# Optimization experiments

Measured on AMD Instinct MI355X. Metric: run time of the kernel, lower is better.

## Reference

```python
import jax, jax.numpy as jnp
import numpy as np

B, S, T, D = 8, 8, 256, 256          # batch, series, time_steps, input_dim
H, DK = 8, 64                         # attn_heads, attn_dim
HD = H * DK                           # 512
L = 2                                 # attn_layers
F = 256                               # mlp_dim
R = 512                               # resolution
M = 128                               # number of mid-points sampled this step
EPS = 1e-5


def setup_inputs() -> dict:
    key = jax.random.key(0)
    ks = iter(jax.random.split(key, 64))

    def rn(shape, scale=0.05):
        return scale * jax.random.normal(next(ks), shape, dtype=jnp.float32)

    inp = {
        'encoded': jax.random.normal(next(ks), (B, S, T, D), dtype=jnp.float32),
        'true_u': jax.random.uniform(next(ks), (B, S, T), dtype=jnp.float32),
        'mid_idx': jnp.sort(jax.random.randint(next(ks), (M,), 0, T)),
        'left_idx': jax.random.randint(next(ks), (M,), 0, T),
        'right_idx': jax.random.randint(next(ks), (M,), 0, T),
        'i': 3,
        # dimension_shift
        'ds_W': rn((D, HD)), 'ds_b': jnp.zeros((HD,), jnp.float32),
        # per-layer, per-head key-creator MLPs (stacked): (D+1) -> F -> F -> DK
        'kW1': rn((L, H, D + 1, F)), 'kb1': jnp.zeros((L, H, F), jnp.float32),
        'kW2': rn((L, H, F, F)),     'kb2': jnp.zeros((L, H, F), jnp.float32),
        'kW3': rn((L, H, F, DK)),    'kb3': jnp.zeros((L, H, DK), jnp.float32),
        # value-creator MLPs
        'vW1': rn((L, H, D + 1, F)), 'vb1': jnp.zeros((L, H, F), jnp.float32),
        'vW2': rn((L, H, F, F)),     'vb2': jnp.zeros((L, H, F), jnp.float32),
        'vW3': rn((L, H, F, DK)),    'vb3': jnp.zeros((L, H, DK), jnp.float32),
        # attention / feed-forward layer norms
        'ln1_g': jnp.ones((L, HD), jnp.float32), 'ln1_b': jnp.zeros((L, HD), jnp.float32),
        'ln2_g': jnp.ones((L, HD), jnp.float32), 'ln2_b': jnp.zeros((L, HD), jnp.float32),
        # feed-forwards
        'ffW1': rn((L, HD, HD)), 'ffb1': jnp.zeros((L, HD), jnp.float32),
        'ffW2': rn((L, HD, HD)), 'ffb2': jnp.zeros((L, HD), jnp.float32),
        # dist_extractors MLP: HD -> F -> F -> R
        'deW1': rn((HD, F)), 'deb1': jnp.zeros((F,), jnp.float32),
        'deW2': rn((F, F)),  'deb2': jnp.zeros((F,), jnp.float32),
        'deW3': rn((F, R)),  'deb3': jnp.zeros((R,), jnp.float32),
    }
    return inp


def _mlp_heads(x, W1, b1, W2, b2, W3, b3):
    # x: [B,S,T,D+1]; weights: [L,H,...] -> out [L,B,S,T,H,DK]
    h = jax.nn.relu(jnp.einsum('bstc,lhcf->lbsthf', x, W1) + b1[:, None, None, None])
    h = jax.nn.relu(jnp.einsum('lbsthf,lhfg->lbsthg', h, W2) + b2[:, None, None, None])
    return jnp.einsum('lbsthg,lhgd->lbsthd', h, W3) + b3[:, None, None, None]


def _ln(x, g, b):
    mu = jnp.mean(x, axis=-1, keepdims=True)
    var = jnp.mean(jnp.square(x - mu), axis=-1, keepdims=True)
    return (x - mu) * jax.lax.rsqrt(var + EPS) * g + b


def reference(encoded, true_u, mid_idx, left_idx, right_idx, i,
              ds_W, ds_b,
              kW1, kb1, kW2, kb2, kW3, kb3,
              vW1, vb1, vW2, vb2, vW3, vb3,
              ln1_g, ln1_b, ln2_g, ln2_b,
              ffW1, ffb1, ffW2, ffb2,
              deW1, deb1, deW2, deb2, deW3, deb3):
    # merged_input = cat([encoded, true_u[..., None]])  -> [B,S,T,D+1]
    merged = jnp.concatenate([encoded, true_u[..., None]], axis=-1)

    keys = _mlp_heads(merged, kW1, kb1, kW2, kb2, kW3, kb3)   # [L,B,S,T,H,DK]
    values = _mlp_heads(merged, vW1, vb1, vW2, vb2, vW3, vb3)  # [L,B,S,T,H,DK]

    srange = jnp.arange(S)
    # n=1 neighbor: time index = loop counter m for series < i, else right[m]
    # (faithful to keys_hist[:, :i, mid:mid+1] in the original)
    idx1 = jnp.where(srange[None, :] < i, jnp.arange(M)[:, None], right_idx[:, None])  # [M,S]

    def gather_neighbors(kv):  # kv: [L,B,S,T,H,DK] -> [L,B,M,S,2,H,DK]
        n0 = jnp.transpose(kv[:, :, :, left_idx], (0, 1, 3, 2, 4, 5))  # [L,B,M,S,H,DK]
        n1 = kv[:, :, srange[None, :], idx1]                            # [L,B,M,S,H,DK]
        return jnp.stack([n0, n1], axis=4)

    nk = gather_neighbors(keys)
    nv = gather_neighbors(values)

    pred = encoded[:, i, mid_idx]                  # [B,M,D]
    att_value = pred @ ds_W + ds_b                 # [B,M,HD]

    scale = DK ** (-0.5)
    for l in range(L):
        avh = att_value.reshape(B, M, H, DK)
        prod = jnp.einsum('bmhd,bmsnhd->bmhsn', avh, nk[l]) * scale
        w = jax.nn.softmax(prod, axis=-1)          # softmax over n only, as in source
        att = jnp.einsum('bmhsn,bmsnhd->bmhd', w, nv[l]).reshape(B, M, HD)
        x = _ln(att_value + att, ln1_g[l], ln1_b[l])
        ff = jax.nn.relu(x @ ffW1[l] + ffb1[l]) @ ffW2[l] + ffb2[l]
        att_value = _ln(x + ff, ln2_g[l], ln2_b[l])

    h = jax.nn.relu(att_value @ deW1 + deb1)
    h = jax.nn.relu(h @ deW2 + deb2)
    logits = h @ deW3 + deb3                       # [B,M,R]
    return logits
```

## Files before the change

### kernel.cpp

```cpp
#include <hip/hip_runtime.h>
#include <hip/hip_bf16.h>

#define NB 8
#define NS 8
#define NT 256
#define ND 256
#define NH 8
#define NDK 64
#define NHD 512
#define NL 2
#define NF 256
#define NR 512
#define NM 128
#define NTOK 16384
#define NROW 1024

typedef __attribute__((ext_vector_type(8))) short short8;
typedef __attribute__((ext_vector_type(4))) float f32x4;

__device__ __forceinline__ unsigned short f2bf(float x) {
    unsigned u = __builtin_bit_cast(unsigned, x);
    unsigned r = (u + 0x7fffu + ((u >> 16) & 1u)) >> 16;
    return (unsigned short)r;
}
__device__ __forceinline__ float bf2f(unsigned short x) {
    return __builtin_bit_cast(float, ((unsigned)x) << 16);
}
__device__ __forceinline__ float wred(float v) {
#pragma unroll
    for (int o = 32; o > 0; o >>= 1) v += __shfl_xor(v, o, 64);
    return v;
}

__global__ __launch_bounds__(256) void prep_all(
    const float* __restrict__ enc,
    const float* __restrict__ kW1, const float* __restrict__ kW2, const float* __restrict__ kW3,
    const float* __restrict__ vW1, const float* __restrict__ vW2, const float* __restrict__ vW3,
    const float* __restrict__ dsW, const float* __restrict__ ffW1,
    const float* __restrict__ ffW2, const float* __restrict__ deW1,
    const float* __restrict__ deW2, const float* __restrict__ deW3,
    unsigned short* __restrict__ XF, unsigned short* __restrict__ WP,
    float* __restrict__ W1L, unsigned short* __restrict__ WG) {
    __shared__ float T[32][257];
    int bid = blockIdx.x, tid = threadIdx.x;
    if (bid < 512) {
        int t0 = bid * 32;
        const float* src = enc + (size_t)t0 * 256;
#pragma unroll
        for (int it = 0; it < 8; ++it) {
            int f4 = it * 256 + tid;
            int row = f4 >> 6, c = (f4 & 63) * 4;
            float4 v = *(const float4*)(src + row * 256 + c);
            T[row][c] = v.x; T[row][c + 1] = v.y; T[row][c + 2] = v.z; T[row][c + 3] = v.w;
        }
        __syncthreads();
        int tile = t0 >> 7, g = (t0 >> 6) & 1, nt0 = (t0 >> 4) & 3;
#pragma unroll
        for (int i = 0; i < 32; i += 8) {
            int o = tid * 32 + i;
            int lane = (o >> 3) & 63, ntp = (o >> 9) & 1, kc = o >> 10;
            int id = lane & 15, quad = lane >> 4;
            __align__(16) unsigned short p[8];
#pragma unroll
            for (int j = 0; j < 8; ++j) p[j] = f2bf(T[ntp * 16 + id][kc * 32 + quad * 8 + j]);
            size_t dsto = ((size_t)((((tile * 8 + kc) * 2 + g) * 4 + (nt0 + ntp)) * 64 + lane)) * 8;
            *(uint4*)(XF + dsto) = *(uint4*)p;
        }
    } else if (bid < 1280) {
        int lb = bid - 512;
        int combo = lb / 24, r = lb % 24;
        int st = r >> 3, kc = r & 7;
        int kvv = combo >> 4, l = (combo >> 3) & 1, h = combo & 7;
        unsigned short* dstc = WP + (size_t)combo * 147456;
        if (st < 2) {
            const float* W = (st == 0) ? (kvv ? vW1 : kW1) : (kvv ? vW2 : kW2);
            int rows = (st == 0) ? 257 : 256;
            const float* src = W + ((size_t)(l * 8 + h) * rows + kc * 32) * 256;
#pragma unroll
            for (int it = 0; it < 8; ++it) {
                int f4 = it * 256 + tid;
                int row = f4 >> 6, c = (f4 & 63) * 4;
                float4 v = *(const float4*)(src + (size_t)row * 256 + c);
                T[row][c] = v.x; T[row][c + 1] = v.y; T[row][c + 2] = v.z; T[row][c + 3] = v.w;
            }
            __syncthreads();
            unsigned short* dst = dstc + st * 65536 + kc * 8192;
#pragma unroll
            for (int i = 0; i < 32; i += 8) {
                int o = tid * 32 + i;
                int lane = (o >> 3) & 63, ftile = o >> 9;
                int id = lane & 15, quad = lane >> 4;
                __align__(16) unsigned short p[8];
#pragma unroll
                for (int j = 0; j < 8; ++j) p[j] = f2bf(T[quad * 8 + j][ftile * 16 + id]);
                *(uint4*)(dst + o) = *(uint4*)p;
            }
            if (st == 0 && kc == 0) {
                const float* hw = (kvv ? vW1 : kW1) + (size_t)(l * 8 + h) * 257 * 256;
                W1L[combo * 256 + tid] = hw[65536 + tid];
            }
        } else {
            const float* src = (kvv ? vW3 : kW3) + ((size_t)(l * 8 + h) * 256 + kc * 32) * 64;
#pragma unroll
            for (int it = 0; it < 2; ++it) {
                int f4 = it * 256 + tid;
                int row = f4 >> 4, c = (f4 & 15) * 4;
                float4 v = *(const float4*)(src + (size_t)row * 64 + c);
                T[row][c] = v.x; T[row][c + 1] = v.y; T[row][c + 2] = v.z; T[row][c + 3] = v.w;
            }
            __syncthreads();
            unsigned short* dst = dstc + 131072 + kc * 2048;
            int o = tid * 8;
            int lane = tid & 63, ftile = tid >> 6;
            int id = lane & 15, quad = lane >> 4;
            __align__(16) unsigned short p[8];
#pragma unroll
            for (int j = 0; j < 8; ++j) p[j] = f2bf(T[quad * 8 + j][ftile * 16 + id]);
            *(uint4*)(dst + o) = *(uint4*)p;
        }
    } else {
        int lb0 = bid - 1280;
        const float* src; int N, kc, ng; size_t base;
        if (lb0 < 32)       { int lb = lb0;       src = dsW;           N = 512; base = 0;       kc = lb >> 2; ng = lb & 3; }
        else if (lb0 < 96)  { int lb = lb0 - 32;  src = ffW1;          N = 512; base = 131072;  kc = lb >> 2; ng = lb & 3; }
        else if (lb0 < 160) { int lb = lb0 - 96;  src = ffW1 + 262144; N = 512; base = 393216;  kc = lb >> 2; ng = lb & 3; }
        else if (lb0 < 224) { int lb = lb0 - 160; src = ffW2;          N = 512; base = 655360;  kc = lb >> 2; ng = lb & 3; }
        else if (lb0 < 288) { int lb = lb0 - 224; src = ffW2 + 262144; N = 512; base = 917504;  kc = lb >> 2; ng = lb & 3; }
        else if (lb0 < 320) { int lb = lb0 - 288; src = deW1;          N = 256; base = 1179648; kc = lb >> 1; ng = lb & 1; }
        else if (lb0 < 336) { int lb = lb0 - 320; src = deW2;          N = 256; base = 1310720; kc = lb >> 1; ng = lb & 1; }
        else                { int lb = lb0 - 336; src = deW3;          N = 512; base = 1376256; kc = lb >> 2; ng = lb & 3; }
        int NTl = N >> 4;
        const float* s = src + (size_t)(kc * 32) * N + ng * 128;
#pragma unroll
        for (int it = 0; it < 4; ++it) {
            int f4 = it * 256 + tid;
            int row = f4 >> 5, c = (f4 & 31) * 4;
            float4 v = *(const float4*)(s + (size_t)row * N + c);
            T[row][c] = v.x; T[row][c + 1] = v.y; T[row][c + 2] = v.z; T[row][c + 3] = v.w;
        }
        __syncthreads();
        unsigned short* d = WG + base + (size_t)(kc * NTl + ng * 8) * 512;
#pragma unroll
        for (int i = 0; i < 16; i += 8) {
            int o = tid * 16 + i;
            int lane = (o >> 3) & 63, ntl = o >> 9;
            int id = lane & 15, quad = lane >> 4;
            __align__(16) unsigned short p[8];
#pragma unroll
            for (int j = 0; j < 8; ++j) p[j] = f2bf(T[quad * 8 + j][ntl * 16 + id]);
            *(uint4*)(d + o) = *(uint4*)p;
        }
    }
}

__global__ __launch_bounds__(256, 4) void heads_mlp(
    const float* __restrict__ tu, const unsigned short* __restrict__ XF,
    const unsigned short* __restrict__ WP, const float* __restrict__ W1L,
    const float* __restrict__ kb1, const float* __restrict__ kb2, const float* __restrict__ kb3,
    const float* __restrict__ vb1, const float* __restrict__ vb2, const float* __restrict__ vb3,
    unsigned short* __restrict__ KV) {
    __shared__ __align__(16) unsigned short smem[16896];

    const int tid = threadIdx.x;
    const int w2 = tid >> 6, lane = tid & 63, id = lane & 15, quad = lane >> 4;
    const int bx = blockIdx.x;
    const int xcd = bx & 7;
    const int idx = bx >> 3;
    const int combo = xcd * 4 + (idx & 3);
    const int t64 = idx >> 2;
    const int kvv = combo >> 4, l = (combo >> 3) & 1, h = combo & 7;
    const int r0 = t64 * 64;
    const int tile128 = t64 >> 1, g = t64 & 1;
    const unsigned short* WF1 = WP + (size_t)combo * 147456;
    const unsigned short* WF2 = WF1 + 65536;
    const unsigned short* WF3 = WF1 + 131072;
    const float* b1 = (kvv ? vb1 : kb1) + (l * 8 + h) * 256;
    const float* b2 = (kvv ? vb2 : kb2) + (l * 8 + h) * 256;
    const float* b3 = (kvv ? vb3 : kb3) + (l * 8 + h) * 64;

    short8 afb[2][4];
#pragma unroll
    for (int ft = 0; ft < 4; ++ft) {
        afb[0][ft] = *(const short8*)(WF1 + (size_t)((w2 * 4 + ft) * 64 + lane) * 8);
        afb[1][ft] = *(const short8*)(WF1 + (size_t)((16 + w2 * 4 + ft) * 64 + lane) * 8);
    }
    {
        const uint4* s = (const uint4*)(XF + (size_t)tile128 * 32768 + g * 2048);
        uint4* d = (uint4*)smem;
#pragma unroll
        for (int kc = 0; kc < 8; ++kc) d[kc * 256 + tid] = s[kc * 512 + tid];
    }
    __syncthreads();

    f32x4 acc[4][4];
#pragma unroll
    for (int i = 0; i < 4; ++i)
#pragma unroll
        for (int j = 0; j < 4; ++j) acc[i][j] = (f32x4){0.f, 0.f, 0.f, 0.f};

    {
#pragma unroll
        for (int kc = 0; kc < 8; ++kc) {
            short8 tn[4];
            if (kc + 2 < 8) {
#pragma unroll
                for (int ft = 0; ft < 4; ++ft)
                    tn[ft] = *(const short8*)(WF1 + (size_t)(((kc + 2) * 16 + w2 * 4 + ft) * 64 + lane) * 8);
            }
            short8 bf[4];
#pragma unroll
            for (int nt = 0; nt < 4; ++nt)
                bf[nt] = *(const short8*)(smem + (size_t)(kc * 4 + nt) * 512 + lane * 8);
#pragma unroll
            for (int ft = 0; ft < 4; ++ft)
#pragma unroll
                for (int nt = 0; nt < 4; ++nt)
                    acc[ft][nt] = __builtin_amdgcn_mfma_f32_16x16x32_bf16(afb[kc & 1][ft], bf[nt], acc[ft][nt], 0, 0, 0);
            if (kc + 2 < 8) {
#pragma unroll
                for (int ft = 0; ft < 4; ++ft) afb[kc & 1][ft] = tn[ft];
            }
        }
    }
    __syncthreads();
    {
        float ur[4];
#pragma unroll
        for (int nt = 0; nt < 4; ++nt) ur[nt] = tu[r0 + nt * 16 + id];
#pragma unroll
        for (int ft = 0; ft < 4; ++ft) {
            int fb = w2 * 64 + ft * 16 + quad * 4;
            float4 bb = *(const float4*)(b1 + fb);
            float4 wl = *(const float4*)(W1L + combo * 256 + fb);
            const float* bbp = (const float*)&bb;
            const float* wlp = (const float*)&wl;
#pragma unroll
            for (int nt = 0; nt < 4; ++nt) {
                unsigned short p[4];
#pragma unroll
                for (int r = 0; r < 4; ++r) {
                    float v = acc[ft][nt][r] + bbp[r] + ur[nt] * wlp[r];
                    p[r] = f2bf(fmaxf(v, 0.f));
                }
                uint2 pk;
                pk.x = (unsigned)p[0] | ((unsigned)p[1] << 16);
                pk.y = (unsigned)p[2] | ((unsigned)p[3] << 16);
                *(uint2*)(smem + (size_t)(nt * 16 + id) * 264 + fb) = pk;
            }
        }
    }
    __syncthreads();

#pragma unroll
    for (int i = 0; i < 4; ++i)
#pragma unroll
        for (int j = 0; j < 4; ++j) acc[i][j] = (f32x4){0.f, 0.f, 0.f, 0.f};
    {
#pragma unroll
        for (int ft = 0; ft < 4; ++ft) {
            afb[0][ft] = *(const short8*)(WF2 + (size_t)((w2 * 4 + ft) * 64 + lane) * 8);
            afb[1][ft] = *(const short8*)(WF2 + (size_t)((16 + w2 * 4 + ft) * 64 + lane) * 8);
        }
#pragma unroll
        for (int kc = 0; kc < 8; ++kc) {
            short8 tn[4];
            if (kc + 2 < 8) {
#pragma unroll
                for (int ft = 0; ft < 4; ++ft)
                    tn[ft] = *(const short8*)(WF2 + (size_t)(((kc + 2) * 16 + w2 * 4 + ft) * 64 + lane) * 8);
            }
            short8 bf[4];
#pragma unroll
            for (int nt = 0; nt < 4; ++nt)
                bf[nt] = *(const short8*)(smem + (size_t)(nt * 16 + id) * 264 + kc * 32 + quad * 8);
#pragma unroll
            for (int ft = 0; ft < 4; ++ft)
#pragma unroll
                for (int nt = 0; nt < 4; ++nt)
                    acc[ft][nt] = __builtin_amdgcn_mfma_f32_16x16x32_bf16(afb[kc & 1][ft], bf[nt], acc[ft][nt], 0, 0, 0);
            if (kc + 2 < 8) {
#pragma unroll
                for (int ft = 0; ft < 4; ++ft) afb[kc & 1][ft] = tn[ft];
            }
        }
    }
    __syncthreads();
#pragma unroll
    for (int ft = 0; ft < 4; ++ft) {
        int fb = w2 * 64 + ft * 16 + quad * 4;
        float4 bb = *(const float4*)(b2 + fb);
        const float* bbp = (const float*)&bb;
#pragma unroll
        for (int nt = 0; nt < 4; ++nt) {
            unsigned short p[4];
#pragma unroll
            for (int r = 0; r < 4; ++r)
                p[r] = f2bf(fmaxf(acc[ft][nt][r] + bbp[r], 0.f));
            uint2 pk;
            pk.x = (unsigned)p[0] | ((unsigned)p[1] << 16);
            pk.y = (unsigned)p[2] | ((unsigned)p[3] << 16);
            *(uint2*)(smem + (size_t)(nt * 16 + id) * 264 + fb) = pk;
        }
    }
    __syncthreads();

    f32x4 a3[4];
#pragma unroll
    for (int i = 0; i < 4; ++i) a3[i] = (f32x4){0.f, 0.f, 0.f, 0.f};
    {
        short8 af3[4], af3n[4];
#pragma unroll
        for (int ft = 0; ft < 4; ++ft)
            af3[ft] = *(const short8*)(WF3 + (size_t)(ft * 64 + lane) * 8);
#pragma unroll
        for (int kc = 0; kc < 8; ++kc) {
            if (kc < 7) {
#pragma unroll
                for (int ft = 0; ft < 4; ++ft)
                    af3n[ft] = *(const short8*)(WF3 + (size_t)(((kc + 1) * 4 + ft) * 64 + lane) * 8);
            }
            short8 b3f = *(const short8*)(smem + (size_t)(w2 * 16 + id) * 264 + kc * 32 + quad * 8);
#pragma unroll
            for (int ft = 0; ft < 4; ++ft)
                a3[ft] = __builtin_amdgcn_mfma_f32_16x16x32_bf16(af3[ft], b3f, a3[ft], 0, 0, 0);
#pragma unroll
            for (int ft = 0; ft < 4; ++ft) af3[ft] = af3n[ft];
        }
    }
    __syncthreads();
    {
        int tl = w2 * 16 + id;
#pragma unroll
        for (int ft = 0; ft < 4; ++ft) {
            int dk0 = ft * 16 + quad * 4;
            float4 bb = *(const float4*)(b3 + dk0);
            const float* bbp = (const float*)&bb;
            unsigned short p[4];
#pragma unroll
            for (int r = 0; r < 4; ++r) p[r] = f2bf(a3[ft][r] + bbp[r]);
            uint2 pk;
            pk.x = (unsigned)p[0] | ((unsigned)p[1] << 16);
            pk.y = (unsigned)p[2] | ((unsigned)p[3] << 16);
            *(uint2*)(smem + (size_t)tl * 72 + dk0) = pk;
        }
    }
    __syncthreads();
    {
#pragma unroll
        for (int it = 0; it < 2; ++it) {
            int tl = it * 32 + (tid >> 3), part = tid & 7;
            uint4 v = *(const uint4*)(smem + (size_t)tl * 72 + part * 8);
            size_t base = ((size_t)combo << 20) + (size_t)(r0 + tl) * 64 + part * 8;
            *(uint4*)(KV + base) = v;
        }
    }
}

__global__ __launch_bounds__(256) void gemm_ds(
    const float* __restrict__ enc, const int* __restrict__ mid,
    const int* __restrict__ ip, const unsigned short* __restrict__ WF,
    const float* __restrict__ bias, float* __restrict__ outf) {
    int tid = threadIdx.x, wv = tid >> 6, lane = tid & 63;
    int id = lane & 15, quad = lane >> 4;
    int ntile = blockIdx.x * 4 + wv;
    int n0 = ntile * 16, m0 = blockIdx.y * 16;
    int iv = ip[0];
    int r0 = m0 + id;
    const float* a0p = enc + (((size_t)((r0 >> 7) * 8 + iv)) * 256 + mid[r0 & 127]) * 256 + quad * 8;
    f32x4 acc0 = (f32x4){0.f, 0.f, 0.f, 0.f};
#pragma unroll
    for (int kc = 0; kc < 8; ++kc) {
        short8 bw = *(const short8*)(WF + (size_t)((kc * 32 + ntile) * 64 + lane) * 8);
        float4 u0 = *(const float4*)(a0p + kc * 32);
        float4 u1 = *(const float4*)(a0p + kc * 32 + 4);
        short8 a0;
        a0[0] = (short)f2bf(u0.x); a0[1] = (short)f2bf(u0.y); a0[2] = (short)f2bf(u0.z); a0[3] = (short)f2bf(u0.w);
        a0[4] = (short)f2bf(u1.x); a0[5] = (short)f2bf(u1.y); a0[6] = (short)f2bf(u1.z); a0[7] = (short)f2bf(u1.w);
        acc0 = __builtin_amdgcn_mfma_f32_16x16x32_bf16(a0, bw, acc0, 0, 0, 0);
    }
    float bv = bias[n0 + id];
#pragma unroll
    for (int r = 0; r < 4; ++r) {
        int row = m0 + quad * 4 + r;
        outf[(size_t)row * 512 + n0 + id] = acc0[r] + bv;
    }
}

__global__ __launch_bounds__(256) void gemm_bf16(
    const unsigned short* __restrict__ A, const unsigned short* __restrict__ WF,
    const float* __restrict__ bias, const float* __restrict__ res,
    float* __restrict__ outf, unsigned short* __restrict__ outb,
    int K, int N, int relu) {
    int tid = threadIdx.x, wv = tid >> 6, lane = tid & 63;
    int id = lane & 15, quad = lane >> 4;
    int ntile = blockIdx.x * 4 + wv;
    int n0 = ntile * 16, m0 = blockIdx.y * 16;
    int NTl = N >> 4, KC = K >> 5;
    f32x4 acc0 = (f32x4){0.f, 0.f, 0.f, 0.f};
    short8 bw = *(const short8*)(WF + (size_t)(ntile * 64 + lane) * 8);
    short8 a0 = *(const short8*)(A + (size_t)(m0 + id) * K + quad * 8);
    for (int kc = 0; kc < KC; ++kc) {
        short8 bwn, a0n;
        if (kc + 1 < KC) {
            bwn = *(const short8*)(WF + (size_t)(((kc + 1) * NTl + ntile) * 64 + lane) * 8);
            a0n = *(const short8*)(A + (size_t)(m0 + id) * K + (kc + 1) * 32 + quad * 8);
        }
        acc0 = __builtin_amdgcn_mfma_f32_16x16x32_bf16(a0, bw, acc0, 0, 0, 0);
        bw = bwn; a0 = a0n;
    }
    float bv = bias[n0 + id];
#pragma unroll
    for (int r = 0; r < 4; ++r) {
        int row = m0 + quad * 4 + r;
        int n = n0 + id;
        float v = acc0[r] + bv;
        if (res) v += res[(size_t)row * N + n];
        if (relu) v = fmaxf(v, 0.f);
        if (outf) outf[(size_t)row * N + n] = v;
        if (outb) outb[(size_t)row * N + n] = f2bf(v);
    }
}

__global__ __launch_bounds__(256) void attn_ln(
    const float* __restrict__ attv, const unsigned short* __restrict__ KV,
    const int* __restrict__ left, const int* __restrict__ right,
    const int* __restrict__ ip,
    const float* __restrict__ g, const float* __restrict__ bb,
    float* __restrict__ xout, unsigned short* __restrict__ xoutb, int l) {
    int tid = threadIdx.x, wv = tid >> 6, lane = tid & 63;
    int gid = blockIdx.x * 4 + wv;
    int b = gid >> 7, m = gid & 127;
    int iv = ip[0];
    int lt = left[m], rt = right[m];
    int h = lane >> 3, d8 = lane & 7;
    const unsigned short* kb = KV + ((size_t)(l * 8 + h) << 20);
    const unsigned short* vb = KV + ((size_t)(16 + l * 8 + h) << 20);
    float av8[8], att8[8];
    {
        const float* avp = attv + (size_t)gid * 512 + lane * 8;
        float4 u0 = *(const float4*)(avp);
        float4 u1 = *(const float4*)(avp + 4);
        av8[0] = u0.x; av8[1] = u0.y; av8[2] = u0.z; av8[3] = u0.w;
        av8[4] = u1.x; av8[5] = u1.y; av8[6] = u1.z; av8[7] = u1.w;
    }
#pragma unroll
    for (int j = 0; j < 8; ++j) att8[j] = 0.f;
#pragma unroll 2
    for (int s = 0; s < 8; ++s) {
        int t1 = (s < iv) ? m : rt;
        size_t o0 = (size_t)((b * 8 + s) * 256 + lt) * 64 + d8 * 8;
        size_t o1 = (size_t)((b * 8 + s) * 256 + t1) * 64 + d8 * 8;
        uint4 k0u = *(const uint4*)(kb + o0);
        uint4 k1u = *(const uint4*)(kb + o1);
        uint4 v0u = *(const uint4*)(vb + o0);
        uint4 v1u = *(const uint4*)(vb + o1);
        const unsigned short* k0 = (const unsigned short*)&k0u;
        const unsigned short* k1 = (const unsigned short*)&k1u;
        const unsigned short* v0 = (const unsigned short*)&v0u;
        const unsigned short* v1 = (const unsigned short*)&v1u;
        float p0 = 0.f, p1 = 0.f;
#pragma unroll
        for (int j = 0; j < 8; ++j) {
            p0 += av8[j] * bf2f(k0[j]);
            p1 += av8[j] * bf2f(k1[j]);
        }
#pragma unroll
        for (int o = 1; o < 8; o <<= 1) {
            p0 += __shfl_xor(p0, o, 64);
            p1 += __shfl_xor(p1, o, 64);
        }
        p0 *= 0.125f; p1 *= 0.125f;
        float mx = fmaxf(p0, p1);
        float e0 = __expf(p0 - mx), e1 = __expf(p1 - mx);
        float inv = 1.f / (e0 + e1);
        float w0 = e0 * inv, w1 = e1 * inv;
#pragma unroll
        for (int j = 0; j < 8; ++j)
            att8[j] += w0 * bf2f(v0[j]) + w1 * bf2f(v1[j]);
    }
    float x8[8], sum = 0.f;
#pragma unroll
    for (int j = 0; j < 8; ++j) { x8[j] = av8[j] + att8[j]; sum += x8[j]; }
    float mu = wred(sum) * (1.f / 512.f);
    float s2 = 0.f;
#pragma unroll
    for (int j = 0; j < 8; ++j) { float d = x8[j] - mu; s2 += d * d; }
    float rs = rsqrtf(wred(s2) * (1.f / 512.f) + 1e-5f);
    {
        const float* gp = g + lane * 8;
        const float* bp = bb + lane * 8;
        float* of = xout + (size_t)gid * 512 + lane * 8;
        unsigned short* ob = xoutb + (size_t)gid * 512 + lane * 8;
        __align__(16) float vout[8];
        __align__(16) unsigned short pb[8];
#pragma unroll
        for (int j = 0; j < 8; ++j) {
            float v = (x8[j] - mu) * rs * gp[j] + bp[j];
            vout[j] = v; pb[j] = f2bf(v);
        }
        *(float4*)(of) = *(float4*)vout;
        *(float4*)(of + 4) = *(float4*)(vout + 4);
        *(uint4*)(ob) = *(uint4*)pb;
    }
}

__global__ __launch_bounds__(256) void ln_k(const float* __restrict__ in,
                                            const float* __restrict__ g,
                                            const float* __restrict__ bb,
                                            float* __restrict__ out,
                                            unsigned short* __restrict__ outb) {
    int tid = threadIdx.x, wv = tid >> 6, lane = tid & 63;
    int gid = blockIdx.x * 4 + wv;
    float x8[8], sum = 0.f;
    {
        const float* ip = in + (size_t)gid * 512 + lane * 8;
        float4 u0 = *(const float4*)(ip);
        float4 u1 = *(const float4*)(ip + 4);
        x8[0] = u0.x; x8[1] = u0.y; x8[2] = u0.z; x8[3] = u0.w;
        x8[4] = u1.x; x8[5] = u1.y; x8[6] = u1.z; x8[7] = u1.w;
    }
#pragma unroll
    for (int j = 0; j < 8; ++j) sum += x8[j];
    float mu = wred(sum) * (1.f / 512.f);
    float s2 = 0.f;
#pragma unroll
    for (int j = 0; j < 8; ++j) { float d = x8[j] - mu; s2 += d * d; }
    float rs = rsqrtf(wred(s2) * (1.f / 512.f) + 1e-5f);
    {
        const float* gp = g + lane * 8;
        const float* bp = bb + lane * 8;
        float* of = out + (size_t)gid * 512 + lane * 8;
        unsigned short* ob = outb + (size_t)gid * 512 + lane * 8;
        __align__(16) float vout[8];
        __align__(16) unsigned short pb[8];
#pragma unroll
        for (int j = 0; j < 8; ++j) {
            float v = (x8[j] - mu) * rs * gp[j] + bp[j];
            vout[j] = v; pb[j] = f2bf(v);
        }
        *(float4*)(of) = *(float4*)vout;
        *(float4*)(of + 4) = *(float4*)(vout + 4);
        *(uint4*)(ob) = *(uint4*)pb;
    }
}

extern "C" void kernel_launch(void* const* d_in, const int* in_sizes, int n_in,
                              void* d_out, int out_size, void* d_ws, size_t ws_size,
                              hipStream_t stream) {
    const float* encoded = (const float*)d_in[0];
    const float* true_u  = (const float*)d_in[1];
    const int* mid_idx   = (const int*)d_in[2];
    const int* left_idx  = (const int*)d_in[3];
    const int* right_idx = (const int*)d_in[4];
    const int* ip        = (const int*)d_in[5];
    const float* ds_W = (const float*)d_in[6];
    const float* ds_b = (const float*)d_in[7];
    const float* kW1 = (const float*)d_in[8];
    const float* kb1 = (const float*)d_in[9];
    const float* kW2 = (const float*)d_in[10];
    const float* kb2 = (const float*)d_in[11];
    const float* kW3 = (const float*)d_in[12];
    const float* kb3 = (const float*)d_in[13];
    const float* vW1 = (const float*)d_in[14];
    const float* vb1 = (const float*)d_in[15];
    const float* vW2 = (const float*)d_in[16];
    const float* vb2 = (const float*)d_in[17];
    const float* vW3 = (const float*)d_in[18];
    const float* vb3 = (const float*)d_in[19];
    const float* ln1_g = (const float*)d_in[20];
    const float* ln1_b = (const float*)d_in[21];
    const float* ln2_g = (const float*)d_in[22];
    const float* ln2_b = (const float*)d_in[23];
    const float* ffW1 = (const float*)d_in[24];
    const float* ffb1 = (const float*)d_in[25];
    const float* ffW2 = (const float*)d_in[26];
    const float* ffb2 = (const float*)d_in[27];
    const float* deW1 = (const float*)d_in[28];
    const float* deb1 = (const float*)d_in[29];
    const float* deW2 = (const float*)d_in[30];
    const float* deb2 = (const float*)d_in[31];
    const float* deW3 = (const float*)d_in[32];
    const float* deb3 = (const float*)d_in[33];

    char* ws = (char*)d_ws;
    unsigned short* XF    = (unsigned short*)(ws + 0);
    unsigned short* WP    = (unsigned short*)(ws + 8388608);
    float* W1L            = (float*)(ws + 17825792);
    unsigned short* KV    = (unsigned short*)(ws + 17858560);
    unsigned short* WG    = (unsigned short*)(ws + 84967424);
    float* ATTV           = (float*)(ws + 87982080);
    float* XBUF           = (float*)(ws + 90079232);
    float* YBUF           = (float*)(ws + 92176384);
    unsigned short* ATTVB = (unsigned short*)(ws + 94273536);
    unsigned short* XBUFB = (unsigned short*)(ws + 95322112);
    unsigned short* FBUFB = (unsigned short*)(ws + 96370688);
    unsigned short* DE1B = XBUFB;
    unsigned short* DE2B = FBUFB;

    unsigned short* WGds    = WG + 0;
    unsigned short* WGff1_0 = WG + 131072;
    unsigned short* WGff1_1 = WG + 393216;
    unsigned short* WGff2_0 = WG + 655360;
    unsigned short* WGff2_1 = WG + 917504;
    unsigned short* WGde1   = WG + 1179648;
    unsigned short* WGde2   = WG + 1310720;
    unsigned short* WGde3   = WG + 1376256;

    prep_all<<<1648, 256, 0, stream>>>(encoded, kW1, kW2, kW3, vW1, vW2, vW3,
                                       ds_W, ffW1, ffW2, deW1, deW2, deW3,
                                       XF, WP, W1L, WG);
    heads_mlp<<<8192, 256, 0, stream>>>(true_u, XF, WP, W1L, kb1, kb2, kb3,
                                        vb1, vb2, vb3, KV);
    gemm_ds<<<dim3(8, 64), 256, 0, stream>>>(encoded, mid_idx, ip, WGds, ds_b, ATTV);
    for (int l = 0; l < 2; ++l) {
        attn_ln<<<256, 256, 0, stream>>>(ATTV, KV, left_idx, right_idx, ip,
                                         ln1_g + l * 512, ln1_b + l * 512,
                                         XBUF, XBUFB, l);
        gemm_bf16<<<dim3(8, 64), 256, 0, stream>>>(XBUFB, (l ? WGff1_1 : WGff1_0),
                                                   ffb1 + l * 512, nullptr,
                                                   nullptr, FBUFB, 512, 512, 1);
        gemm_bf16<<<dim3(8, 64), 256, 0, stream>>>(FBUFB, (l ? WGff2_1 : WGff2_0),
                                                   ffb2 + l * 512, XBUF,
                                                   YBUF, nullptr, 512, 512, 0);
        ln_k<<<256, 256, 0, stream>>>(YBUF, ln2_g + l * 512, ln2_b + l * 512, ATTV, ATTVB);
    }
    gemm_bf16<<<dim3(4, 64), 256, 0, stream>>>(ATTVB, WGde1, deb1, nullptr,
                                               nullptr, DE1B, 512, 256, 1);
    gemm_bf16<<<dim3(4, 64), 256, 0, stream>>>(DE1B, WGde2, deb2, nullptr,
                                               nullptr, DE2B, 256, 256, 1);
    gemm_bf16<<<dim3(8, 64), 256, 0, stream>>>(DE2B, WGde3, deb3, nullptr,
                                               (float*)d_out, nullptr, 256, 512, 0);
}
```

Baseline: 421.1 us.

## Double heads_mlp token tile to 128 with 512 threads and swizzled LDS

```diff
diff --git a/kernel.cpp b/kernel.cpp
--- a/kernel.cpp
+++ b/kernel.cpp
@@ -30,6 +30,11 @@
 #pragma unroll
     for (int o = 32; o > 0; o >>= 1) v += __shfl_xor(v, o, 64);
     return v;
+}
+
+__device__ __forceinline__ int SW(int row, int scol) {
+    int g = (scol >> 2) ^ ((row & 7) << 3);
+    return row * 256 + g * 4 + (scol & 3);
 }
 
 __global__ __launch_bounds__(256) void prep_all(
@@ -153,24 +158,38 @@
     }
 }
 
-__global__ __launch_bounds__(256, 4) void heads_mlp(
+#define LDW(S, DST)                                                                              \
+    do {                                                                                         \
+        if ((S) < 8) {                                                                           \
+            _Pragma("unroll") for (int ft_ = 0; ft_ < 4; ++ft_)                                  \
+                (DST)[ft_] = *(const short8*)(WF1 + (size_t)(((S) * 16 + wf * 4 + ft_) * 64 + lane) * 8); \
+        } else if ((S) < 16) {                                                                   \
+            _Pragma("unroll") for (int ft_ = 0; ft_ < 4; ++ft_)                                  \
+                (DST)[ft_] = *(const short8*)(WF2 + (size_t)((((S) - 8) * 16 + wf * 4 + ft_) * 64 + lane) * 8); \
+        } else if ((S) < 24) {                                                                   \
+            _Pragma("unroll") for (int ft_ = 0; ft_ < 4; ++ft_)                                  \
+                (DST)[ft_] = *(const short8*)(WF3 + (size_t)((((S) - 16) * 4 + ft_) * 64 + lane) * 8); \
+        }                                                                                        \
+    } while (0)
+
+__global__ __launch_bounds__(512, 4) void heads_mlp(
     const float* __restrict__ tu, const unsigned short* __restrict__ XF,
     const unsigned short* __restrict__ WP, const float* __restrict__ W1L,
     const float* __restrict__ kb1, const float* __restrict__ kb2, const float* __restrict__ kb3,
     const float* __restrict__ vb1, const float* __restrict__ vb2, const float* __restrict__ vb3,
     unsigned short* __restrict__ KV) {
-    __shared__ __align__(16) unsigned short smem[16896];
+    __shared__ __align__(16) unsigned short smem[32768];
 
     const int tid = threadIdx.x;
-    const int w2 = tid >> 6, lane = tid & 63, id = lane & 15, quad = lane >> 4;
+    const int wave = tid >> 6, lane = tid & 63, id = lane & 15, quad = lane >> 4;
+    const int wf = wave & 3, wt = wave >> 2;
     const int bx = blockIdx.x;
     const int xcd = bx & 7;
     const int idx = bx >> 3;
     const int combo = xcd * 4 + (idx & 3);
-    const int t64 = idx >> 2;
+    const int t128 = idx >> 2;
     const int kvv = combo >> 4, l = (combo >> 3) & 1, h = combo & 7;
-    const int r0 = t64 * 64;
-    const int tile128 = t64 >> 1, g = t64 & 1;
+    const int r0 = t128 * 128;
     const unsigned short* WF1 = WP + (size_t)combo * 147456;
     const unsigned short* WF2 = WF1 + 65536;
     const unsigned short* WF3 = WF1 + 131072;
@@ -179,16 +198,13 @@
     const float* b3 = (kvv ? vb3 : kb3) + (l * 8 + h) * 64;
 
     short8 afb[2][4];
-#pragma unroll
-    for (int ft = 0; ft < 4; ++ft) {
-        afb[0][ft] = *(const short8*)(WF1 + (size_t)((w2 * 4 + ft) * 64 + lane) * 8);
-        afb[1][ft] = *(const short8*)(WF1 + (size_t)((16 + w2 * 4 + ft) * 64 + lane) * 8);
-    }
-    {
-        const uint4* s = (const uint4*)(XF + (size_t)tile128 * 32768 + g * 2048);
+    LDW(0, afb[0]);
+    LDW(1, afb[1]);
+    {
+        const uint4* s = (const uint4*)(XF + (size_t)t128 * 32768);
         uint4* d = (uint4*)smem;
 #pragma unroll
-        for (int kc = 0; kc < 8; ++kc) d[kc * 256 + tid] = s[kc * 512 + tid];
+        for (int it = 0; it < 8; ++it) d[it * 512 + tid] = s[it * 512 + tid];
     }
     __syncthreads();
 
@@ -198,44 +214,37 @@
 #pragma unroll
         for (int j = 0; j < 4; ++j) acc[i][j] = (f32x4){0.f, 0.f, 0.f, 0.f};
 
-    {
-#pragma unroll
-        for (int kc = 0; kc < 8; ++kc) {
-            short8 tn[4];
-            if (kc + 2 < 8) {
-#pragma unroll
-                for (int ft = 0; ft < 4; ++ft)
-                    tn[ft] = *(const short8*)(WF1 + (size_t)(((kc + 2) * 16 + w2 * 4 + ft) * 64 + lane) * 8);
-            }
-            short8 bf[4];
+#pragma unroll
+    for (int kc = 0; kc < 8; ++kc) {
+        short8 tn[4];
+        LDW(kc + 2, tn);
+        short8 bf[4];
+#pragma unroll
+        for (int nt = 0; nt < 4; ++nt)
+            bf[nt] = *(const short8*)(smem + (size_t)(kc * 8 + wt * 4 + nt) * 512 + lane * 8);
+#pragma unroll
+        for (int ft = 0; ft < 4; ++ft)
 #pragma unroll
             for (int nt = 0; nt < 4; ++nt)
-                bf[nt] = *(const short8*)(smem + (size_t)(kc * 4 + nt) * 512 + lane * 8);
-#pragma unroll
-            for (int ft = 0; ft < 4; ++ft)
-#pragma unroll
-                for (int nt = 0; nt < 4; ++nt)
-                    acc[ft][nt] = __builtin_amdgcn_mfma_f32_16x16x32_bf16(afb[kc & 1][ft], bf[nt], acc[ft][nt], 0, 0, 0);
-            if (kc + 2 < 8) {
-#pragma unroll
-                for (int ft = 0; ft < 4; ++ft) afb[kc & 1][ft] = tn[ft];
-            }
-        }
+                acc[ft][nt] = __builtin_amdgcn_mfma_f32_16x16x32_bf16(afb[kc & 1][ft], bf[nt], acc[ft][nt], 0, 0, 0);
+#pragma unroll
+        for (int ft = 0; ft < 4; ++ft) afb[kc & 1][ft] = tn[ft];
     }
     __syncthreads();
     {
         float ur[4];
 #pragma unroll
-        for (int nt = 0; nt < 4; ++nt) ur[nt] = tu[r0 + nt * 16 + id];
+        for (int nt = 0; nt < 4; ++nt) ur[nt] = tu[r0 + wt * 64 + nt * 16 + id];
 #pragma unroll
         for (int ft = 0; ft < 4; ++ft) {
-            int fb = w2 * 64 + ft * 16 + quad * 4;
+            int fb = wf * 64 + ft * 16 + quad * 4;
             float4 bb = *(const float4*)(b1 + fb);
             float4 wl = *(const float4*)(W1L + combo * 256 + fb);
             const float* bbp = (const float*)&bb;
             const float* wlp = (const float*)&wl;
 #pragma unroll
             for (int nt = 0; nt < 4; ++nt) {
+                int row = wt * 64 + nt * 16 + id;
                 unsigned short p[4];
 #pragma unroll
                 for (int r = 0; r < 4; ++r) {
@@ -245,7 +254,7 @@
                 uint2 pk;
                 pk.x = (unsigned)p[0] | ((unsigned)p[1] << 16);
                 pk.y = (unsigned)p[2] | ((unsigned)p[3] << 16);
-                *(uint2*)(smem + (size_t)(nt * 16 + id) * 264 + fb) = pk;
+                *(uint2*)(smem + SW(row, fb)) = pk;
             }
         }
     }
@@ -255,43 +264,31 @@
     for (int i = 0; i < 4; ++i)
 #pragma unroll
         for (int j = 0; j < 4; ++j) acc[i][j] = (f32x4){0.f, 0.f, 0.f, 0.f};
-    {
-#pragma unroll
-        for (int ft = 0; ft < 4; ++ft) {
-            afb[0][ft] = *(const short8*)(WF2 + (size_t)((w2 * 4 + ft) * 64 + lane) * 8);
-            afb[1][ft] = *(const short8*)(WF2 + (size_t)((16 + w2 * 4 + ft) * 64 + lane) * 8);
-        }
-#pragma unroll
-        for (int kc = 0; kc < 8; ++kc) {
-            short8 tn[4];
-            if (kc + 2 < 8) {
-#pragma unroll
-                for (int ft = 0; ft < 4; ++ft)
-                    tn[ft] = *(const short8*)(WF2 + (size_t)(((kc + 2) * 16 + w2 * 4 + ft) * 64 + lane) * 8);
-            }
-            short8 bf[4];
+#pragma unroll
+    for (int kc = 0; kc < 8; ++kc) {
+        short8 tn[4];
+        LDW(kc + 10, tn);
+        short8 bf[4];
+#pragma unroll
+        for (int nt = 0; nt < 4; ++nt)
+            bf[nt] = *(const short8*)(smem + SW(wt * 64 + nt * 16 + id, kc * 32 + quad * 8));
+#pragma unroll
+        for (int ft = 0; ft < 4; ++ft)
 #pragma unroll
             for (int nt = 0; nt < 4; ++nt)
-                bf[nt] = *(const short8*)(smem + (size_t)(nt * 16 + id) * 264 + kc * 32 + quad * 8);
-#pragma unroll
-            for (int ft = 0; ft < 4; ++ft)
-#pragma unroll
-                for (int nt = 0; nt < 4; ++nt)
-                    acc[ft][nt] = __builtin_amdgcn_mfma_f32_16x16x32_bf16(afb[kc & 1][ft], bf[nt], acc[ft][nt], 0, 0, 0);
-            if (kc + 2 < 8) {
-#pragma unroll
-                for (int ft = 0; ft < 4; ++ft) afb[kc & 1][ft] = tn[ft];
-            }
-        }
+                acc[ft][nt] = __builtin_amdgcn_mfma_f32_16x16x32_bf16(afb[kc & 1][ft], bf[nt], acc[ft][nt], 0, 0, 0);
+#pragma unroll
+        for (int ft = 0; ft < 4; ++ft) afb[kc & 1][ft] = tn[ft];
     }
     __syncthreads();
 #pragma unroll
     for (int ft = 0; ft < 4; ++ft) {
-        int fb = w2 * 64 + ft * 16 + quad * 4;
+        int fb = wf * 64 + ft * 16 + quad * 4;
         float4 bb = *(const float4*)(b2 + fb);
         const float* bbp = (const float*)&bb;
 #pragma unroll
         for (int nt = 0; nt < 4; ++nt) {
+            int row = wt * 64 + nt * 16 + id;
             unsigned short p[4];
 #pragma unroll
             for (int r = 0; r < 4; ++r)
@@ -299,7 +296,7 @@
             uint2 pk;
             pk.x = (unsigned)p[0] | ((unsigned)p[1] << 16);
             pk.y = (unsigned)p[2] | ((unsigned)p[3] << 16);
-            *(uint2*)(smem + (size_t)(nt * 16 + id) * 264 + fb) = pk;
+            *(uint2*)(smem + SW(row, fb)) = pk;
         }
     }
     __syncthreads();
@@ -307,29 +304,22 @@
     f32x4 a3[4];
 #pragma unroll
     for (int i = 0; i < 4; ++i) a3[i] = (f32x4){0.f, 0.f, 0.f, 0.f};
-    {
-        short8 af3[4], af3n[4];
+#pragma unroll
+    for (int kc = 0; kc < 8; ++kc) {
+        short8 tn[4];
+        if (kc + 18 < 24) LDW(kc + 18, tn);
+        short8 b3f = *(const short8*)(smem + SW(wave * 16 + id, kc * 32 + quad * 8));
 #pragma unroll
         for (int ft = 0; ft < 4; ++ft)
-            af3[ft] = *(const short8*)(WF3 + (size_t)(ft * 64 + lane) * 8);
-#pragma unroll
-        for (int kc = 0; kc < 8; ++kc) {
-            if (kc < 7) {
-#pragma unroll
-                for (int ft = 0; ft < 4; ++ft)
-                    af3n[ft] = *(const short8*)(WF3 + (size_t)(((kc + 1) * 4 + ft) * 64 + lane) * 8);
-            }
-            short8 b3f = *(const short8*)(smem + (size_t)(w2 * 16 + id) * 264 + kc * 32 + quad * 8);
-#pragma unroll
-            for (int ft = 0; ft < 4; ++ft)
-                a3[ft] = __builtin_amdgcn_mfma_f32_16x16x32_bf16(af3[ft], b3f, a3[ft], 0, 0, 0);
-#pragma unroll
-            for (int ft = 0; ft < 4; ++ft) af3[ft] = af3n[ft];
+            a3[ft] = __builtin_amdgcn_mfma_f32_16x16x32_bf16(afb[kc & 1][ft], b3f, a3[ft], 0, 0, 0);
+        if (kc + 18 < 24) {
+#pragma unroll
+            for (int ft = 0; ft < 4; ++ft) afb[kc & 1][ft] = tn[ft];
         }
     }
     __syncthreads();
     {
-        int tl = w2 * 16 + id;
+        int tl = wave * 16 + id;
 #pragma unroll
         for (int ft = 0; ft < 4; ++ft) {
             int dk0 = ft * 16 + quad * 4;
@@ -348,7 +338,7 @@
     {
 #pragma unroll
         for (int it = 0; it < 2; ++it) {
-            int tl = it * 32 + (tid >> 3), part = tid & 7;
+            int tl = it * 64 + (tid >> 3), part = tid & 7;
             uint4 v = *(const uint4*)(smem + (size_t)tl * 72 + part * 8);
             size_t base = ((size_t)combo << 20) + (size_t)(r0 + tl) * 64 + part * 8;
             *(uint4*)(KV + base) = v;
@@ -609,7 +599,7 @@
     prep_all<<<1648, 256, 0, stream>>>(encoded, kW1, kW2, kW3, vW1, vW2, vW3,
                                        ds_W, ffW1, ffW2, deW1, deW2, deW3,
                                        XF, WP, W1L, WG);
-    heads_mlp<<<8192, 256, 0, stream>>>(true_u, XF, WP, W1L, kb1, kb2, kb3,
+    heads_mlp<<<4096, 512, 0, stream>>>(true_u, XF, WP, W1L, kb1, kb2, kb3,
                                         vb1, vb2, vb3, KV);
     gemm_ds<<<dim3(8, 64), 256, 0, stream>>>(encoded, mid_idx, ip, WGds, ds_b, ATTV);
     for (int l = 0; l < 2; ++l) {
```

New measurement: 452.5 us. 7.5% more time.
